# Kernel tuning notes

Measured on AMD Instinct MI355X. Metric: run time of the kernel, lower is better.

The kernel has to match this reference:

```python
import jax, jax.numpy as jnp
import numpy as np

B, T, E, H = 64, 200, 512, 8
D = E // H          # head size 64
SCALE = E ** -0.5   # NOTE: original scales by EMBED_DIM**-0.5, not head_size**-0.5


def _ln(x, g, b):
    mu = jnp.mean(x, axis=-1, keepdims=True)
    d = x - mu
    v = jnp.mean(d * d, axis=-1, keepdims=True)
    return g * d * jax.lax.rsqrt(v + 1e-5) + b


def _forward(idx, memory, src_mask, pred_mask,
             sa_wq, sa_wk, sa_wv, sa_wo, sa_bo,
             ca_wq, ca_wk, ca_wv, ca_wo, ca_bo,
             f_w1, f_b1, f_w2, f_b2,
             ln1_g, ln1_b, ln2_g, ln2_b, ln3_g, ln3_b):
    causal = jnp.tril(jnp.ones((T, T), dtype=bool))      # [T,T]
    pm = (pred_mask != 0)[:, None, :, None]              # [B,1,T,1]
    sm = (src_mask != 0)[:, None, :, None]               # [B,1,T,1]

    # --- masked multi-head self-attention (query AND key zeroed by pred_mask) ---
    h = _ln(idx, ln1_g, ln1_b)
    q = jnp.where(pm, jnp.einsum('bte,hed->bhtd', h, sa_wq), 0.0)
    k = jnp.where(pm, jnp.einsum('bte,hed->bhtd', h, sa_wk), 0.0)
    v = jnp.einsum('bte,hed->bhtd', h, sa_wv)
    s = jnp.einsum('bhtd,bhsd->bhts', q, k) * SCALE
    s = jnp.where(causal, s, -jnp.inf)
    w = jax.nn.softmax(s, axis=-1)
    o = jnp.einsum('bhts,bhsd->bthd', w, v).reshape(B, T, E)
    idx = o @ sa_wo + sa_bo + idx

    # --- cross-attention: keys from memory (src-masked), VALUES FROM x (per original code) ---
    h = _ln(idx, ln2_g, ln2_b)
    q = jnp.einsum('bte,hed->bhtd', h, ca_wq)
    k = jnp.where(sm, jnp.einsum('bse,hed->bhsd', memory, ca_wk), 0.0)
    v = jnp.einsum('bte,hed->bhtd', h, ca_wv)
    s = jnp.einsum('bhtd,bhsd->bhts', q, k) * SCALE
    s = jnp.where(causal, s, -jnp.inf)   # mask=True in Decoder's ca
    w = jax.nn.softmax(s, axis=-1)
    o = jnp.einsum('bhts,bhsd->bthd', w, v).reshape(B, T, E)
    idx = o @ ca_wo + ca_bo + idx

    # --- feed-forward ---
    h = _ln(idx, ln3_g, ln3_b)
    idx = jax.nn.relu(h @ f_w1 + f_b1) @ f_w2 + f_b2 + idx
    return idx


def setup_inputs() -> dict:
    key = jax.random.key(0)
    ks = jax.random.split(key, 20)
    nrm = lambda k, sh: jax.random.normal(k, sh, jnp.float32) * 0.02
    return {
        'idx': jax.random.normal(ks[0], (B, T, E), jnp.float32),
        'memory': jax.random.normal(ks[1], (B, T, E), jnp.float32),
        'src_mask': jax.random.randint(ks[2], (B, T), 0, 2, jnp.int32),
        'pred_mask': jax.random.randint(ks[3], (B, T), 0, 2, jnp.int32),
        'sa_wq': nrm(ks[4], (H, E, D)), 'sa_wk': nrm(ks[5], (H, E, D)),
        'sa_wv': nrm(ks[6], (H, E, D)),
        'sa_wo': nrm(ks[7], (E, E)), 'sa_bo': jnp.zeros((E,), jnp.float32),
        'ca_wq': nrm(ks[8], (H, E, D)), 'ca_wk': nrm(ks[9], (H, E, D)),
        'ca_wv': nrm(ks[10], (H, E, D)),
        'ca_wo': nrm(ks[11], (E, E)), 'ca_bo': jnp.zeros((E,), jnp.float32),
        'f_w1': nrm(ks[12], (E, 4 * E)), 'f_b1': jnp.zeros((4 * E,), jnp.float32),
        'f_w2': nrm(ks[13], (4 * E, E)), 'f_b2': jnp.zeros((E,), jnp.float32),
        'ln1_g': jnp.ones((E,), jnp.float32), 'ln1_b': jnp.zeros((E,), jnp.float32),
        'ln2_g': jnp.ones((E,), jnp.float32), 'ln2_b': jnp.zeros((E,), jnp.float32),
        'ln3_g': jnp.ones((E,), jnp.float32), 'ln3_b': jnp.zeros((E,), jnp.float32),
    }


def reference(idx, memory, src_mask, pred_mask,
              sa_wq, sa_wk, sa_wv, sa_wo, sa_bo,
              ca_wq, ca_wk, ca_wv, ca_wo, ca_bo,
              f_w1, f_b1, f_w2, f_b2,
              ln1_g, ln1_b, ln2_g, ln2_b, ln3_g, ln3_b):
    return _forward(idx, memory, src_mask, pred_mask,
                    sa_wq, sa_wk, sa_wv, sa_wo, sa_bo,
                    ca_wq, ca_wk, ca_wv, ca_wo, ca_bo,
                    f_w1, f_b1, f_w2, f_b2,
                    ln1_g, ln1_b, ln2_g, ln2_b, ln3_g, ln3_b)
```

## Files before the change

### kernel.cpp

```cpp
#include <hip/hip_runtime.h>
#include <hip/hip_bf16.h>

#define B_ 64
#define T_ 200
#define E_ 512
#define H_ 8
#define D_ 64

static constexpr float SCALE = 0.044194173824159216f;

typedef __attribute__((ext_vector_type(8))) short bf16x8;
typedef __attribute__((ext_vector_type(4))) short bf16x4;
typedef __attribute__((ext_vector_type(4))) float f32x4;

static __device__ inline short f2bf(float f) {
    __hip_bfloat16 h = __float2bfloat16(f);
    return *(short*)&h;
}

static __device__ __forceinline__ void gload16(const short* g, short* l) {
    __builtin_amdgcn_global_load_lds(
        (const __attribute__((address_space(1))) void*)g,
        (__attribute__((address_space(3))) void*)l, 16, 0, 0);
}

__global__ void conv_kernel(const float* __restrict__ in,
                            __hip_bfloat16* __restrict__ out, int n) {
    int i = (blockIdx.x * blockDim.x + threadIdx.x) * 4;
    if (i < n) {
        f32x4 v = *(const f32x4*)(in + i);
        bf16x4 r;
        #pragma unroll
        for (int j = 0; j < 4; ++j) r[j] = f2bf(v[j]);
        *(bf16x4*)((short*)out + i) = r;
    }
}

template <int MODE>
__global__ __launch_bounds__(256) void wt_kernel(const float* __restrict__ in,
                                                 __hip_bfloat16* __restrict__ out,
                                                 int N, int K) {
    __shared__ float tile[64][65];
    int n0 = blockIdx.x * 64, k0 = blockIdx.y * 64;
    int tx = threadIdx.x & 63, ty = threadIdx.x >> 6;
    #pragma unroll
    for (int i = 0; i < 16; ++i) {
        int k = k0 + ty + i * 4;
        float v;
        if (MODE == 0) {
            v = in[(size_t)k * N + n0 + tx];
        } else {
            int h = n0 >> 6;
            v = in[((size_t)h * K + k) * 64 + tx];
        }
        tile[ty + i * 4][tx] = v;
    }
    __syncthreads();
    #pragma unroll
    for (int i = 0; i < 16; ++i) {
        int n = ty + i * 4;
        out[(size_t)(n0 + n) * K + k0 + tx] = __float2bfloat16(tile[tx][n]);
    }
}

__global__ __launch_bounds__(256) void ln_kernel(const float* __restrict__ x,
                                                 const float* __restrict__ g,
                                                 const float* __restrict__ bta,
                                                 __hip_bfloat16* __restrict__ out) {
    __shared__ float red[4];
    int row = blockIdx.x;
    const float* xr = x + (size_t)row * E_;
    int tid = threadIdx.x;
    float v0 = xr[tid], v1 = xr[tid + 256];
    float s = v0 + v1;
    for (int off = 32; off; off >>= 1) s += __shfl_down(s, off, 64);
    if ((tid & 63) == 0) red[tid >> 6] = s;
    __syncthreads();
    float mu = (red[0] + red[1] + red[2] + red[3]) * (1.0f / E_);
    __syncthreads();
    float d0 = v0 - mu, d1 = v1 - mu;
    float sq = d0 * d0 + d1 * d1;
    for (int off = 32; off; off >>= 1) sq += __shfl_down(sq, off, 64);
    if ((tid & 63) == 0) red[tid >> 6] = sq;
    __syncthreads();
    float var = (red[0] + red[1] + red[2] + red[3]) * (1.0f / E_);
    float r = rsqrtf(var + 1e-5f);
    out[(size_t)row * E_ + tid] = __float2bfloat16(g[tid] * d0 * r + bta[tid]);
    out[(size_t)row * E_ + tid + 256] =
        __float2bfloat16(g[tid + 256] * d1 * r + bta[tid + 256]);
}

template <int MSK, int RELU, int OM, int RES, int BIAS>
__global__ __launch_bounds__(256) void mgemm_kernel(
    const short* __restrict__ A, const short* __restrict__ A2,
    const short* __restrict__ BT,
    const float* __restrict__ bias, const int* __restrict__ rmask,
    const float* __restrict__ resid, void* __restrict__ Cv,
    int M, int N, int K, size_t wstep) {
    __shared__ __align__(16) short As[2][128 * 64];
    __shared__ __align__(16) short Bs[2][128 * 64];
    int tid = threadIdx.x;
    int wave = tid >> 6, lane = tid & 63;
    int qq = lane >> 4, l15 = lane & 15;

    int nwg = gridDim.x * gridDim.y;
    int flat = blockIdx.y * gridDim.x + blockIdx.x;
    int xcd = flat & 7, bix = flat >> 3;
    int qw = nwg >> 3, rw = nwg & 7;
    int nf = (xcd < rw ? xcd * (qw + 1) : rw * (qw + 1) + (xcd - rw) * qw) + bix;
    int by = nf / gridDim.x, bx = nf - by * gridDim.x;
    int m0 = by * 128, n0 = bx * 128;
    int wm = (wave & 1) * 64, wn = (wave >> 1) * 64;

    const short* Ap = A;
    if (OM == 4 && n0 >= 1024) Ap = A2;

    int srow = lane >> 3;
    int scol = ((lane & 7) ^ srow) * 8;
    const short* gA = Ap + (size_t)(m0 + wave * 32 + srow) * K + scol;
    const short* gB = BT + (size_t)(n0 + wave * 32 + srow) * K + scol;
    int lofs = wave * 32 * 64;
    size_t rstep = (size_t)8 * K;

    f32x4 acc[4][4] = {};

    auto STAGE = [&](int kt, int bufi) {
        int kk = kt << 6;
        #pragma unroll
        for (int c = 0; c < 4; ++c) {
            gload16(gA + kk + c * rstep, &As[bufi][lofs + c * 512]);
            gload16(gB + kk + c * rstep, &Bs[bufi][lofs + c * 512]);
        }
    };

    int nk = K >> 6;
    STAGE(0, 0);

    for (int it = 0; it < nk; ++it) {
        int cur = it & 1;
        if (it + 1 < nk) {
            STAGE(it + 1, cur ^ 1);
            asm volatile("s_waitcnt vmcnt(8)" ::: "memory");
        } else {
            asm volatile("s_waitcnt vmcnt(0)" ::: "memory");
        }
        __builtin_amdgcn_s_barrier();
        bf16x8 af[2][4], bfr[2][4];
        #pragma unroll
        for (int ks = 0; ks < 2; ++ks) {
            int pu = ((ks * 4 + qq) ^ (l15 & 7)) * 8;
            #pragma unroll
            for (int i = 0; i < 4; ++i)
                af[ks][i] = *(bf16x8*)(&As[cur][(wm + i * 16 + l15) * 64 + pu]);
            #pragma unroll
            for (int j = 0; j < 4; ++j)
                bfr[ks][j] = *(bf16x8*)(&Bs[cur][(wn + j * 16 + l15) * 64 + pu]);
        }
        #pragma unroll
        for (int ks = 0; ks < 2; ++ks)
            #pragma unroll
            for (int i = 0; i < 4; ++i)
                #pragma unroll
                for (int j = 0; j < 4; ++j)
                    acc[i][j] = __builtin_amdgcn_mfma_f32_16x16x32_bf16(
                        af[ks][i], bfr[ks][j], acc[i][j], 0, 0, 0);
        asm volatile("" ::: "memory");
        __builtin_amdgcn_s_barrier();
    }

    #pragma unroll
    for (int i = 0; i < 4; ++i) {
        #pragma unroll
        for (int r = 0; r < 4; ++r) {
            int row = m0 + wm + i * 16 + qq * 4 + r;
            float mval = 1.0f;
            if (MSK) mval = (rmask[row] != 0) ? 1.0f : 0.0f;
            #pragma unroll
            for (int j = 0; j < 4; ++j) {
                int col = n0 + wn + j * 16 + l15;
                float val = acc[i][j][r];
                if (BIAS) val += bias[col];
                if (MSK == 1) val *= mval;
                if (MSK == 2) { if (col < 1024) val *= mval; }
                if (MSK == 3) { if (col >= 1024) val *= mval; }
                if (RELU) val = fmaxf(val, 0.0f);
                if (RES) val += resid[(size_t)row * N + col];
                if (OM == 0) {
                    ((float*)Cv)[(size_t)row * N + col] = val;
                } else if (OM == 3) {
                    int b_ = row / T_, t = row - b_ * T_;
                    int which = col >> 9, cc = col & 511;
                    int hh = cc >> 6, d = cc & 63;
                    ((__hip_bfloat16*)Cv)[(size_t)which * wstep +
                                          (((size_t)b_ * H_ + hh) * T_ + t) * D_ + d] =
                        __float2bfloat16(val);
                } else if (OM == 4) {
                    int b_ = row / T_, t = row - b_ * T_;
                    int which = col >> 9, cc = col & 511;
                    size_t off = (which == 1) ? 2 * wstep : (which == 2 ? wstep : 0);
                    int hh = cc >> 6, d = cc & 63;
                    ((__hip_bfloat16*)Cv)[off +
                                          (((size_t)b_ * H_ + hh) * T_ + t) * D_ + d] =
                        __float2bfloat16(val);
                } else {
                    ((__hip_bfloat16*)Cv)[(size_t)row * N + col] =
                        __float2bfloat16(val);
                }
            }
        }
    }
}

#define NQT 13
__global__ __launch_bounds__(256) void fattn_kernel(const short* __restrict__ q,
                                                    const short* __restrict__ k,
                                                    const short* __restrict__ v,
                                                    __hip_bfloat16* __restrict__ o) {
    __shared__ __align__(16) short Kf[NQT * 8 * 16 * 8];
    __shared__ __align__(16) short Vf[4 * 28 * 16 * 8];
    __shared__ __align__(16) short Pb[4 * 512];

    int tid = threadIdx.x;
    int wave = tid >> 6, lane = tid & 63;
    int qq = lane >> 4, l15 = lane & 15;
    int bh = blockIdx.x;
    int b = bh >> 3, h = bh & 7;

    const short* kp = k + (size_t)bh * T_ * D_;
    const short* vp = v + (size_t)bh * T_ * D_;
    const short* qp = q + (size_t)bh * T_ * D_;

    for (int idx = tid; idx < 8 * 208; idx += 256) {
        int g = idx / 208, s = idx - g * 208;
        int kt = s >> 4, l = s & 15;
        bf16x8 val;
        if (s < 200) {
            val = *(const bf16x8*)(kp + (size_t)s * 64 + g * 8);
        } else {
            #pragma unroll
            for (int j = 0; j < 8; ++j) val[j] = 0;
        }
        *(bf16x8*)&Kf[((kt * 8 + g) * 16 + l) * 8] = val;
    }
    for (int idx = tid; idx < 28 * 64; idx += 256) {
        int g = idx >> 6, d = idx & 63;
        int nt = d >> 4, dl = d & 15;
        bf16x8 val;
        if (g < 25) {
            #pragma unroll
            for (int j = 0; j < 8; ++j) val[j] = vp[(g * 8 + j) * 64 + d];
        } else {
            #pragma unroll
            for (int j = 0; j < 8; ++j) val[j] = 0;
        }
        *(bf16x8*)&Vf[((nt * 28 + g) * 16 + dl) * 8] = val;
    }
    __syncthreads();

    short* pb = &Pb[wave * 512];

    for (int qt = wave; qt < NQT; qt += 4) {
        int t0 = qt * 16;
        bf16x8 qf[2];
        #pragma unroll
        for (int ks = 0; ks < 2; ++ks)
            qf[ks] = *(const bf16x8*)(qp + (size_t)(t0 + l15) * 64 + ks * 32 + qq * 8);
        f32x4 sc[NQT];
        #pragma unroll
        for (int kt = 0; kt < NQT; ++kt) {
            f32x4 a = {0.f, 0.f, 0.f, 0.f};
            bf16x8 kf0 = *(const bf16x8*)&Kf[((kt * 8 + qq) * 16 + l15) * 8];
            bf16x8 kf1 = *(const bf16x8*)&Kf[((kt * 8 + 4 + qq) * 16 + l15) * 8];
            a = __builtin_amdgcn_mfma_f32_16x16x32_bf16(qf[0], kf0, a, 0, 0, 0);
            a = __builtin_amdgcn_mfma_f32_16x16x32_bf16(qf[1], kf1, a, 0, 0, 0);
            sc[kt] = a;
        }
        #pragma unroll
        for (int kt = 0; kt < NQT; ++kt) {
            #pragma unroll
            for (int r = 0; r < 4; ++r) {
                int col = kt * 16 + l15;
                int rowg = t0 + qq * 4 + r;
                sc[kt][r] = (col <= rowg) ? sc[kt][r] * SCALE : -1e30f;
            }
        }
        float mx[4], sum[4], inv[4];
        #pragma unroll
        for (int r = 0; r < 4; ++r) {
            float m = -1e30f;
            #pragma unroll
            for (int kt = 0; kt < NQT; ++kt) m = fmaxf(m, sc[kt][r]);
            #pragma unroll
            for (int off = 1; off < 16; off <<= 1)
                m = fmaxf(m, __shfl_xor(m, off, 64));
            mx[r] = m;
        }
        #pragma unroll
        for (int r = 0; r < 4; ++r) sum[r] = 0.f;
        #pragma unroll
        for (int kt = 0; kt < NQT; ++kt) {
            #pragma unroll
            for (int r = 0; r < 4; ++r) {
                float e = __expf(sc[kt][r] - mx[r]);
                sc[kt][r] = e;
                sum[r] += e;
            }
        }
        #pragma unroll
        for (int r = 0; r < 4; ++r) {
            float s = sum[r];
            #pragma unroll
            for (int off = 1; off < 16; off <<= 1) s += __shfl_xor(s, off, 64);
            inv[r] = 1.0f / s;
        }
        f32x4 oa[4] = {};
        #pragma unroll
        for (int c = 0; c < 7; ++c) {
            #pragma unroll
            for (int kt2 = 0; kt2 < 2; ++kt2) {
                int kt = c * 2 + kt2;
                int g = kt2 * 2 + (l15 >> 3);
                int jj = l15 & 7;
                #pragma unroll
                for (int r = 0; r < 4; ++r) {
                    float val = (kt < NQT) ? sc[kt][r] : 0.0f;
                    pb[(g * 16 + qq * 4 + r) * 8 + jj] = f2bf(val);
                }
            }
            bf16x8 pf = *(const bf16x8*)&pb[(qq * 16 + l15) * 8];
            #pragma unroll
            for (int nt = 0; nt < 4; ++nt) {
                bf16x8 vf = *(const bf16x8*)&Vf[((nt * 28 + c * 4 + qq) * 16 + l15) * 8];
                oa[nt] = __builtin_amdgcn_mfma_f32_16x16x32_bf16(pf, vf, oa[nt], 0, 0, 0);
            }
        }
        #pragma unroll
        for (int nt = 0; nt < 4; ++nt) {
            #pragma unroll
            for (int r = 0; r < 4; ++r) {
                int t = t0 + qq * 4 + r;
                if (t < T_) {
                    int d = nt * 16 + l15;
                    o[((size_t)b * T_ + t) * E_ + h * D_ + d] =
                        __float2bfloat16(oa[nt][r] * inv[r]);
                }
            }
        }
    }
}

extern "C" void kernel_launch(void* const* d_in, const int* in_sizes, int n_in,
                              void* d_out, int out_size, void* d_ws, size_t ws_size,
                              hipStream_t stream) {
    const float* idx    = (const float*)d_in[0];
    const float* memory = (const float*)d_in[1];
    const int* src_mask  = (const int*)d_in[2];
    const int* pred_mask = (const int*)d_in[3];
    const float* sa_wq = (const float*)d_in[4];
    const float* sa_wk = (const float*)d_in[5];
    const float* sa_wv = (const float*)d_in[6];
    const float* sa_wo = (const float*)d_in[7];
    const float* sa_bo = (const float*)d_in[8];
    const float* ca_wq = (const float*)d_in[9];
    const float* ca_wk = (const float*)d_in[10];
    const float* ca_wv = (const float*)d_in[11];
    const float* ca_wo = (const float*)d_in[12];
    const float* ca_bo = (const float*)d_in[13];
    const float* f_w1  = (const float*)d_in[14];
    const float* f_b1  = (const float*)d_in[15];
    const float* f_w2  = (const float*)d_in[16];
    const float* f_b2  = (const float*)d_in[17];
    const float* ln1_g = (const float*)d_in[18];
    const float* ln1_b = (const float*)d_in[19];
    const float* ln2_g = (const float*)d_in[20];
    const float* ln2_b = (const float*)d_in[21];
    const float* ln3_g = (const float*)d_in[22];
    const float* ln3_b = (const float*)d_in[23];
    float* out = (float*)d_out;

    const size_t BTE = (size_t)B_ * T_ * E_;
    const size_t EE = (size_t)E_ * E_;

    char* p = (char*)d_ws;
    short* qb = (short*)p;            p += BTE * 2;
    short* kb = (short*)p;            p += BTE * 2;
    short* vb = (short*)p;            p += BTE * 2;
    float* x1 = (float*)p;            p += BTE * 4;
    __hip_bfloat16* h_bf   = (__hip_bfloat16*)p; p += BTE * 2;
    __hip_bfloat16* o_bf   = (__hip_bfloat16*)p; p += BTE * 2;
    __hip_bfloat16* mem_bf = (__hip_bfloat16*)p; p += BTE * 2;
    __hip_bfloat16* w_qkv_s = (__hip_bfloat16*)p; p += 3 * EE * 2;
    __hip_bfloat16* w_o_s   = (__hip_bfloat16*)p; p += EE * 2;
    __hip_bfloat16* w_qvk_c = (__hip_bfloat16*)p; p += 3 * EE * 2;
    __hip_bfloat16* w_o_c   = (__hip_bfloat16*)p; p += EE * 2;
    __hip_bfloat16* w1T     = (__hip_bfloat16*)p; p += EE * 4 * 2;
    __hip_bfloat16* w2T     = (__hip_bfloat16*)p; p += EE * 4 * 2;
    short* ff_bf = qb;

    const int M = B_ * T_;
    dim3 blk(256);
    dim3 g512(E_ / 128, M / 128);
    dim3 g1536(12, M / 128);
    dim3 g2048(16, M / 128);

    dim3 t512(8, 8), t_w1(32, 8), t_w2(8, 32);
    wt_kernel<1><<<t512, blk, 0, stream>>>(sa_wq, w_qkv_s, E_, E_);
    wt_kernel<1><<<t512, blk, 0, stream>>>(sa_wk, w_qkv_s + EE, E_, E_);
    wt_kernel<1><<<t512, blk, 0, stream>>>(sa_wv, w_qkv_s + 2 * EE, E_, E_);
    wt_kernel<0><<<t512, blk, 0, stream>>>(sa_wo, w_o_s, E_, E_);
    wt_kernel<1><<<t512, blk, 0, stream>>>(ca_wq, w_qvk_c, E_, E_);
    wt_kernel<1><<<t512, blk, 0, stream>>>(ca_wv, w_qvk_c + EE, E_, E_);
    wt_kernel<1><<<t512, blk, 0, stream>>>(ca_wk, w_qvk_c + 2 * EE, E_, E_);
    wt_kernel<0><<<t512, blk, 0, stream>>>(ca_wo, w_o_c, E_, E_);
    wt_kernel<0><<<t_w1, blk, 0, stream>>>(f_w1, w1T, 4 * E_, E_);
    wt_kernel<0><<<t_w2, blk, 0, stream>>>(f_w2, w2T, E_, 4 * E_);
    conv_kernel<<<((int)(BTE / 4) + 255) / 256, 256, 0, stream>>>(memory, mem_bf,
                                                                  (int)BTE);

    ln_kernel<<<M, 256, 0, stream>>>(idx, ln1_g, ln1_b, h_bf);
    mgemm_kernel<2,0,3,0,0><<<g1536, blk, 0, stream>>>(
        (const short*)h_bf, nullptr, (const short*)w_qkv_s, nullptr, pred_mask,
        nullptr, qb, M, 3 * E_, E_, BTE);
    fattn_kernel<<<B_ * H_, 256, 0, stream>>>(qb, kb, vb, o_bf);
    mgemm_kernel<0,0,0,1,1><<<g512, blk, 0, stream>>>(
        (const short*)o_bf, nullptr, (const short*)w_o_s, sa_bo, nullptr, idx, x1,
        M, E_, E_, 0);

    ln_kernel<<<M, 256, 0, stream>>>(x1, ln2_g, ln2_b, h_bf);
    mgemm_kernel<3,0,4,0,0><<<g1536, blk, 0, stream>>>(
        (const short*)h_bf, (const short*)mem_bf, (const short*)w_qvk_c, nullptr,
        src_mask, nullptr, qb, M, 3 * E_, E_, BTE);
    fattn_kernel<<<B_ * H_, 256, 0, stream>>>(qb, kb, vb, o_bf);
    mgemm_kernel<0,0,0,1,1><<<g512, blk, 0, stream>>>(
        (const short*)o_bf, nullptr, (const short*)w_o_c, ca_bo, nullptr, x1, out,
        M, E_, E_, 0);

    ln_kernel<<<M, 256, 0, stream>>>(out, ln3_g, ln3_b, h_bf);
    mgemm_kernel<0,1,2,0,1><<<g2048, blk, 0, stream>>>(
        (const short*)h_bf, nullptr, (const short*)w1T, f_b1, nullptr, nullptr,
        ff_bf, M, 4 * E_, E_, 0);
    mgemm_kernel<0,0,0,1,1><<<g512, blk, 0, stream>>>(
        (const short*)ff_bf, nullptr, (const short*)w2T, f_b2, nullptr, out, out,
        M, E_, 4 * E_, 0);
}
```

Baseline: 435.3 us.

## Skip masked causal tiles in attention, balance waves, and fuse weight transposes

The attention kernel now skips key tiles above the causal diagonal for each query tile. Each wave is given a hand-picked set of query tiles so the triangular work is spread evenly across waves. The ten separate weight-transpose launches are merged into one kernel that picks its source and destination by block index, cutting launch overhead. The GEMM epilogue is moved into a helper function with the mask lookup now done per element, and the wave-to-tile table is hardcoded for 13 query tiles.

New measurement: 453.9 us. +4.3%, slower.

```diff
diff --git a/kernel.cpp b/kernel.cpp
--- a/kernel.cpp
+++ b/kernel.cpp
@@ -23,6 +23,9 @@
         (const __attribute__((address_space(1))) void*)g,
         (__attribute__((address_space(3))) void*)l, 16, 0, 0);
 }
+
+#define FENCE asm volatile("" ::: "memory")
+#define VMCNT(n) asm volatile("s_waitcnt vmcnt(" #n ")" ::: "memory")
 
 __global__ void conv_kernel(const float* __restrict__ in,
                             __hip_bfloat16* __restrict__ out, int n) {
@@ -36,23 +39,49 @@
     }
 }
 
-template <int MODE>
-__global__ __launch_bounds__(256) void wt_kernel(const float* __restrict__ in,
-                                                 __hip_bfloat16* __restrict__ out,
-                                                 int N, int K) {
+__global__ __launch_bounds__(256) void wtall_kernel(
+    const float* s0, const float* s1, const float* s2, const float* s3,
+    const float* s4, const float* s5, const float* s6, const float* s7,
+    const float* s8, const float* s9,
+    __hip_bfloat16* d0, __hip_bfloat16* d1, __hip_bfloat16* d2,
+    __hip_bfloat16* d3, __hip_bfloat16* d4, __hip_bfloat16* d5,
+    __hip_bfloat16* d6, __hip_bfloat16* d7, __hip_bfloat16* d8,
+    __hip_bfloat16* d9) {
     __shared__ float tile[64][65];
-    int n0 = blockIdx.x * 64, k0 = blockIdx.y * 64;
+    int id = blockIdx.x;
+    const float* in;
+    __hip_bfloat16* out;
+    int N = 512, K = 512, mode = 1, nb, kb;
+    if (id < 512) {
+        int z = id >> 6, r = id & 63;
+        nb = r & 7; kb = r >> 3;
+        switch (z) {
+            case 0: in = s0; out = d0; break;
+            case 1: in = s1; out = d1; break;
+            case 2: in = s2; out = d2; break;
+            case 3: in = s3; out = d3; mode = 0; break;
+            case 4: in = s4; out = d4; break;
+            case 5: in = s5; out = d5; break;
+            case 6: in = s6; out = d6; break;
+            default: in = s7; out = d7; mode = 0; break;
+        }
+    } else if (id < 768) {
+        int r = id - 512;
+        in = s8; out = d8; mode = 0; N = 2048;
+        nb = r & 31; kb = r >> 5;
+    } else {
+        int r = id - 768;
+        in = s9; out = d9; mode = 0; K = 2048;
+        nb = r & 7; kb = r >> 3;
+    }
+    int n0 = nb * 64, k0 = kb * 64;
     int tx = threadIdx.x & 63, ty = threadIdx.x >> 6;
     #pragma unroll
     for (int i = 0; i < 16; ++i) {
         int k = k0 + ty + i * 4;
         float v;
-        if (MODE == 0) {
-            v = in[(size_t)k * N + n0 + tx];
-        } else {
-            int h = n0 >> 6;
-            v = in[((size_t)h * K + k) * 64 + tx];
-        }
+        if (mode == 0) v = in[(size_t)k * N + n0 + tx];
+        else { int h = n0 >> 6; v = in[((size_t)h * K + k) * 64 + tx]; }
         tile[ty + i * 4][tx] = v;
     }
     __syncthreads();
@@ -91,6 +120,40 @@
 }
 
 template <int MSK, int RELU, int OM, int RES, int BIAS>
+static __device__ __forceinline__ void epi_store(
+    float val, int row, int col, int N, size_t wstep,
+    const float* bias, const int* rmask, const float* resid, void* Cv) {
+    if (BIAS) val += bias[col];
+    if (MSK) {
+        float mval = (rmask[row] != 0) ? 1.0f : 0.0f;
+        if (MSK == 1) val *= mval;
+        if (MSK == 2) { if (col < 1024) val *= mval; }
+        if (MSK == 3) { if (col >= 1024) val *= mval; }
+    }
+    if (RELU) val = fmaxf(val, 0.0f);
+    if (RES) val += resid[(size_t)row * N + col];
+    if (OM == 0) {
+        ((float*)Cv)[(size_t)row * N + col] = val;
+    } else if (OM == 3) {
+        int b_ = row / T_, t = row - b_ * T_;
+        int which = col >> 9, cc = col & 511;
+        int hh = cc >> 6, d = cc & 63;
+        ((__hip_bfloat16*)Cv)[(size_t)which * wstep +
+                              (((size_t)b_ * H_ + hh) * T_ + t) * D_ + d] =
+            __float2bfloat16(val);
+    } else if (OM == 4) {
+        int b_ = row / T_, t = row - b_ * T_;
+        int which = col >> 9, cc = col & 511;
+        size_t off = (which == 1) ? 2 * wstep : (which == 2 ? wstep : 0);
+        int hh = cc >> 6, d = cc & 63;
+        ((__hip_bfloat16*)Cv)[off + (((size_t)b_ * H_ + hh) * T_ + t) * D_ + d] =
+            __float2bfloat16(val);
+    } else {
+        ((__hip_bfloat16*)Cv)[(size_t)row * N + col] = __float2bfloat16(val);
+    }
+}
+
+template <int MSK, int RELU, int OM, int RES, int BIAS>
 __global__ __launch_bounds__(256) void mgemm_kernel(
     const short* __restrict__ A, const short* __restrict__ A2,
     const short* __restrict__ BT,
@@ -140,9 +203,9 @@
         int cur = it & 1;
         if (it + 1 < nk) {
             STAGE(it + 1, cur ^ 1);
-            asm volatile("s_waitcnt vmcnt(8)" ::: "memory");
+            VMCNT(8);
         } else {
-            asm volatile("s_waitcnt vmcnt(0)" ::: "memory");
+            VMCNT(0);
         }
         __builtin_amdgcn_s_barrier();
         bf16x8 af[2][4], bfr[2][4];
@@ -164,51 +227,22 @@
                 for (int j = 0; j < 4; ++j)
                     acc[i][j] = __builtin_amdgcn_mfma_f32_16x16x32_bf16(
                         af[ks][i], bfr[ks][j], acc[i][j], 0, 0, 0);
-        asm volatile("" ::: "memory");
+        FENCE;
         __builtin_amdgcn_s_barrier();
     }
 
     #pragma unroll
-    for (int i = 0; i < 4; ++i) {
+    for (int i = 0; i < 4; ++i)
         #pragma unroll
         for (int r = 0; r < 4; ++r) {
             int row = m0 + wm + i * 16 + qq * 4 + r;
-            float mval = 1.0f;
-            if (MSK) mval = (rmask[row] != 0) ? 1.0f : 0.0f;
             #pragma unroll
             for (int j = 0; j < 4; ++j) {
                 int col = n0 + wn + j * 16 + l15;
-                float val = acc[i][j][r];
-                if (BIAS) val += bias[col];
-                if (MSK == 1) val *= mval;
-                if (MSK == 2) { if (col < 1024) val *= mval; }
-                if (MSK == 3) { if (col >= 1024) val *= mval; }
-                if (RELU) val = fmaxf(val, 0.0f);
-                if (RES) val += resid[(size_t)row * N + col];
-                if (OM == 0) {
-                    ((float*)Cv)[(size_t)row * N + col] = val;
-                } else if (OM == 3) {
-                    int b_ = row / T_, t = row - b_ * T_;
-                    int which = col >> 9, cc = col & 511;
-                    int hh = cc >> 6, d = cc & 63;
-                    ((__hip_bfloat16*)Cv)[(size_t)which * wstep +
-                                          (((size_t)b_ * H_ + hh) * T_ + t) * D_ + d] =
-                        __float2bfloat16(val);
-                } else if (OM == 4) {
-                    int b_ = row / T_, t = row - b_ * T_;
-                    int which = col >> 9, cc = col & 511;
-                    size_t off = (which == 1) ? 2 * wstep : (which == 2 ? wstep : 0);
-                    int hh = cc >> 6, d = cc & 63;
-                    ((__hip_bfloat16*)Cv)[off +
-                                          (((size_t)b_ * H_ + hh) * T_ + t) * D_ + d] =
-                        __float2bfloat16(val);
-                } else {
-                    ((__hip_bfloat16*)Cv)[(size_t)row * N + col] =
-                        __float2bfloat16(val);
-                }
-            }
-        }
-    }
+                epi_store<MSK, RELU, OM, RES, BIAS>(acc[i][j][r], row, col, N,
+                                                    wstep, bias, rmask, resid, Cv);
+            }
+        }
 }
 
 #define NQT 13
@@ -259,7 +293,13 @@
 
     short* pb = &Pb[wave * 512];
 
-    for (int qt = wave; qt < NQT; qt += 4) {
+    unsigned pk = (wave == 0) ? 0xF35Cu : (wave == 1) ? 0xF26Bu
+                : (wave == 2) ? 0x017Au : 0xF489u;
+
+    #pragma unroll 1
+    for (int s = 0; s < 4; ++s) {
+        int qt = (pk >> (4 * s)) & 15;
+        if (qt == 15) break;
         int t0 = qt * 16;
         bf16x8 qf[2];
         #pragma unroll
@@ -268,6 +308,7 @@
         f32x4 sc[NQT];
         #pragma unroll
         for (int kt = 0; kt < NQT; ++kt) {
+            if (kt > qt) continue;
             f32x4 a = {0.f, 0.f, 0.f, 0.f};
             bf16x8 kf0 = *(const bf16x8*)&Kf[((kt * 8 + qq) * 16 + l15) * 8];
             bf16x8 kf1 = *(const bf16x8*)&Kf[((kt * 8 + 4 + qq) * 16 + l15) * 8];
@@ -277,6 +318,7 @@
         }
         #pragma unroll
         for (int kt = 0; kt < NQT; ++kt) {
+            if (kt > qt) continue;
             #pragma unroll
             for (int r = 0; r < 4; ++r) {
                 int col = kt * 16 + l15;
@@ -289,7 +331,10 @@
         for (int r = 0; r < 4; ++r) {
             float m = -1e30f;
             #pragma unroll
-            for (int kt = 0; kt < NQT; ++kt) m = fmaxf(m, sc[kt][r]);
+            for (int kt = 0; kt < NQT; ++kt) {
+                if (kt > qt) continue;
+                m = fmaxf(m, sc[kt][r]);
+            }
             #pragma unroll
             for (int off = 1; off < 16; off <<= 1)
                 m = fmaxf(m, __shfl_xor(m, off, 64));
@@ -299,6 +344,7 @@
         for (int r = 0; r < 4; ++r) sum[r] = 0.f;
         #pragma unroll
         for (int kt = 0; kt < NQT; ++kt) {
+            if (kt > qt) continue;
             #pragma unroll
             for (int r = 0; r < 4; ++r) {
                 float e = __expf(sc[kt][r] - mx[r]);
@@ -308,14 +354,15 @@
         }
         #pragma unroll
         for (int r = 0; r < 4; ++r) {
-            float s = sum[r];
-            #pragma unroll
-            for (int off = 1; off < 16; off <<= 1) s += __shfl_xor(s, off, 64);
-            inv[r] = 1.0f / s;
+            float s2 = sum[r];
+            #pragma unroll
+            for (int off = 1; off < 16; off <<= 1) s2 += __shfl_xor(s2, off, 64);
+            inv[r] = 1.0f / s2;
         }
         f32x4 oa[4] = {};
         #pragma unroll
         for (int c = 0; c < 7; ++c) {
+            if (2 * c > qt) continue;
             #pragma unroll
             for (int kt2 = 0; kt2 < 2; ++kt2) {
                 int kt = c * 2 + kt2;
@@ -323,7 +370,7 @@
                 int jj = l15 & 7;
                 #pragma unroll
                 for (int r = 0; r < 4; ++r) {
-                    float val = (kt < NQT) ? sc[kt][r] : 0.0f;
+                    float val = (kt <= qt) ? sc[kt][r] : 0.0f;
                     pb[(g * 16 + qq * 4 + r) * 8 + jj] = f2bf(val);
                 }
             }
@@ -335,7 +382,7 @@
             }
         }
         #pragma unroll
-        for (int nt = 0; nt < 4; ++nt) {
+        for (int nt = 0; nt < 4; ++nt)
             #pragma unroll
             for (int r = 0; r < 4; ++r) {
                 int t = t0 + qq * 4 + r;
@@ -345,7 +392,6 @@
                         __float2bfloat16(oa[nt][r] * inv[r]);
                 }
             }
-        }
     }
 }
 
@@ -403,17 +449,10 @@
     dim3 g1536(12, M / 128);
     dim3 g2048(16, M / 128);
 
-    dim3 t512(8, 8), t_w1(32, 8), t_w2(8, 32);
-    wt_kernel<1><<<t512, blk, 0, stream>>>(sa_wq, w_qkv_s, E_, E_);
-    wt_kernel<1><<<t512, blk, 0, stream>>>(sa_wk, w_qkv_s + EE, E_, E_);
-    wt_kernel<1><<<t512, blk, 0, stream>>>(sa_wv, w_qkv_s + 2 * EE, E_, E_);
-    wt_kernel<0><<<t512, blk, 0, stream>>>(sa_wo, w_o_s, E_, E_);
-    wt_kernel<1><<<t512, blk, 0, stream>>>(ca_wq, w_qvk_c, E_, E_);
-    wt_kernel<1><<<t512, blk, 0, stream>>>(ca_wv, w_qvk_c + EE, E_, E_);
-    wt_kernel<1><<<t512, blk, 0, stream>>>(ca_wk, w_qvk_c + 2 * EE, E_, E_);
-    wt_kernel<0><<<t512, blk, 0, stream>>>(ca_wo, w_o_c, E_, E_);
-    wt_kernel<0><<<t_w1, blk, 0, stream>>>(f_w1, w1T, 4 * E_, E_);
-    wt_kernel<0><<<t_w2, blk, 0, stream>>>(f_w2, w2T, E_, 4 * E_);
+    wtall_kernel<<<1024, blk, 0, stream>>>(
+        sa_wq, sa_wk, sa_wv, sa_wo, ca_wq, ca_wv, ca_wk, ca_wo, f_w1, f_w2,
+        w_qkv_s, w_qkv_s + EE, w_qkv_s + 2 * EE, w_o_s,
+        w_qvk_c, w_qvk_c + EE, w_qvk_c + 2 * EE, w_o_c, w1T, w2T);
     conv_kernel<<<((int)(BTE / 4) + 255) / 256, 256, 0, stream>>>(memory, mem_bf,
                                                                   (int)BTE);
 
```
